# Optimization experiments

Measured on AMD Instinct MI355X. Metric: run time of the kernel, lower is better.

Reference implementation:

```python
import jax, jax.numpy as jnp
import numpy as np

M = 4096  # rows (axis -2), cosine transform axis
N = 4096  # cols (axis -1), sine transform axis


def setup_inputs() -> dict:
    key = jax.random.key(0)
    x = jax.random.normal(key, (M, N), dtype=jnp.float32)
    return {"x": x}


def _cos_basis(n):
    # C[u, p] = cos(pi * (2u+1) * p / (2n))  -- IDXCT basis (no coefficient normalization)
    u = jnp.arange(n, dtype=jnp.float32)
    p = jnp.arange(n, dtype=jnp.float32)
    return jnp.cos(jnp.pi * (2.0 * u[:, None] + 1.0) * p[None, :] / (2.0 * n))


def _sin_basis(n):
    # S[v, q] = sin(pi * (2v+1) * q / (2n))  -- IDXST basis (q=0 column is zero)
    v = jnp.arange(n, dtype=jnp.float32)
    q = jnp.arange(n, dtype=jnp.float32)
    return jnp.sin(jnp.pi * (2.0 * v[:, None] + 1.0) * q[None, :] / (2.0 * n))


def reference(x):
    # idcst2(x) = idxct(idxst(x)^T)^T
    # y_{u,v} = sum_p sum_q x_{p,q} * cos(pi*p*(2u+1)/(2M)) * sin(pi*q*(2v+1)/(2N))
    m, n = x.shape[-2], x.shape[-1]
    C0 = _cos_basis(m).astype(x.dtype)  # [M, M]
    S1 = _sin_basis(n).astype(x.dtype)  # [N, N]
    y = jnp.matmul(x, S1.T)   # IDXST along last axis: [M, N]
    out = jnp.matmul(C0, y)   # IDXCT along axis -2:  [M, N]
    return out
```

## Files before the change

### kernel.cpp

```cpp
#include <hip/hip_runtime.h>


#define NF 4096
#define TWOPI_16384 3.8349519697141029e-4f
#define TWOPI_4096  1.5339807878856412e-3f
#define TWOPI_256   2.4543692606170259e-2f

__device__ __forceinline__ float2 cmul(float2 a, float2 b) {
    return make_float2(a.x * b.x - a.y * b.y, a.x * b.y + a.y * b.x);
}
__device__ __forceinline__ float2 cadd(float2 a, float2 b) {
    return make_float2(a.x + b.x, a.y + b.y);
}
__device__ __forceinline__ float2 csub(float2 a, float2 b) {
    return make_float2(a.x - b.x, a.y - b.y);
}
__device__ __forceinline__ float2 muli(float2 a) {
    return make_float2(-a.y, a.x);
}

__device__ __forceinline__ void fft16(float2 f[16]) {
    float2 s[16];
#pragma unroll
    for (int b = 0; b < 4; ++b) {
        float2 x0 = f[b], x1 = f[b + 4], x2 = f[b + 8], x3 = f[b + 12];
        float2 t0 = cadd(x0, x2), t1 = csub(x0, x2);
        float2 t2 = cadd(x1, x3), t3 = csub(x1, x3);
        s[b]      = cadd(t0, t2);
        s[4 + b]  = cadd(t1, muli(t3));
        s[8 + b]  = csub(t0, t2);
        s[12 + b] = csub(t1, muli(t3));
    }
    const float2 w1 = make_float2(0.92387953251128674f, 0.38268343236508977f);
    const float2 w2 = make_float2(0.70710678118654752f, 0.70710678118654752f);
    const float2 w3 = make_float2(0.38268343236508977f, 0.92387953251128674f);
    const float2 w6 = make_float2(-0.70710678118654752f, 0.70710678118654752f);
    const float2 w9 = make_float2(-0.92387953251128674f, -0.38268343236508977f);
    s[5]  = cmul(s[5], w1);
    s[6]  = cmul(s[6], w2);
    s[7]  = cmul(s[7], w3);
    s[9]  = cmul(s[9], w2);
    s[10] = muli(s[10]);
    s[11] = cmul(s[11], w6);
    s[13] = cmul(s[13], w3);
    s[14] = cmul(s[14], w6);
    s[15] = cmul(s[15], w9);
#pragma unroll
    for (int al = 0; al < 4; ++al) {
        float2 x0 = s[4 * al + 0], x1 = s[4 * al + 1];
        float2 x2 = s[4 * al + 2], x3 = s[4 * al + 3];
        float2 t0 = cadd(x0, x2), t1 = csub(x0, x2);
        float2 t2 = cadd(x1, x3), t3 = csub(x1, x3);
        f[al]      = cadd(t0, t2);
        f[4 + al]  = cadd(t1, muli(t3));
        f[8 + al]  = csub(t0, t2);
        f[12 + al] = csub(t1, muli(t3));
    }
}

__device__ __forceinline__ void fft4096_r16(float2* __restrict__ buf, const int t) {
    float2 r[16];
#pragma unroll
    for (int i = 0; i < 16; ++i) r[i] = buf[i * 256 + t];
    fft16(r);
    {
        float sn, cs;
        __sincosf((float)t * TWOPI_4096, &sn, &cs);
        const float2 wb = make_float2(cs, sn);
        float2 w = wb;
#pragma unroll
        for (int k1 = 1; k1 < 16; ++k1) { r[k1] = cmul(r[k1], w); w = cmul(w, wb); }
    }
#pragma unroll
    for (int i = 0; i < 16; ++i) buf[i * 256 + t] = r[i];
    __syncthreads();
    {
        const int k1 = t >> 4, m2 = t & 15;
        const int base = k1 * 256 + m2;
#pragma unroll
        for (int i = 0; i < 16; ++i) r[i] = buf[base + i * 16];
        fft16(r);
        float sn, cs;
        __sincosf((float)m2 * TWOPI_256, &sn, &cs);
        const float2 wb = make_float2(cs, sn);
        float2 w = wb;
#pragma unroll
        for (int j1 = 1; j1 < 16; ++j1) { r[j1] = cmul(r[j1], w); w = cmul(w, wb); }
        __syncthreads();
        const int bw = k1 * 256 + (m2 ^ k1);
#pragma unroll
        for (int j1 = 0; j1 < 16; ++j1) buf[bw + j1 * 16] = r[j1];
    }
    __syncthreads();
    {
        const int k1 = t & 15;
        const int bc = k1 * 256 + (t >> 4) * 16;
#pragma unroll
        for (int i = 0; i < 16; ++i) r[i] = buf[bc + (i ^ k1)];
        fft16(r);
        __syncthreads();
#pragma unroll
        for (int j2 = 0; j2 < 16; ++j2) buf[j2 * 256 + t] = r[j2];
    }
    __syncthreads();
}

__global__ __launch_bounds__(256) void dst_rows_k(const float* __restrict__ x,
                                                  float* __restrict__ y) {
    __shared__ float2 buf[4096];
    const int t = threadIdx.x;
    const size_t r0 = (size_t)blockIdx.x * 2;
    const float* x0 = x + r0 * NF;
    const float* x1 = x0 + NF;

    float sn, cs;
    __sincosf((float)t * TWOPI_16384, &sn, &cs);
    float2 w = make_float2(cs, sn);
    const float2 stp = make_float2(0.99518472667219693f, 0.09801714032956060f);
#pragma unroll
    for (int v = 0; v < 16; ++v) {
        const int k = t + 256 * v;
        float2 ww = make_float2(0.f, 0.f);
        if (k > 0) {
            float re = x0[NF - k] + x1[k];
            float im = x1[NF - k] - x0[k];
            ww = make_float2(re * w.x - im * w.y, re * w.y + im * w.x);
        }
        buf[k] = ww;
        w = cmul(w, stp);
    }

    fft4096_r16(buf, t);

    float* y0 = y + r0 * NF;
    float* y1 = y0 + NF;
#pragma unroll
    for (int u = 0; u < 8; ++u) {
        const int n = t + 256 * u;
        float2 vn = buf[n];
        float2 vm = buf[NF - 1 - n];
        ((float2*)y0)[n] = make_float2(0.5f * vn.x, -0.5f * vm.x);
        ((float2*)y1)[n] = make_float2(0.5f * vn.y, -0.5f * vm.y);
    }
}

__global__ __launch_bounds__(256) void dct_rows_k(const float* __restrict__ yt,
                                                  float* __restrict__ ot) {
    __shared__ float2 buf[4096];
    const int t = threadIdx.x;
    const size_t r0 = (size_t)blockIdx.x * 2;
    const float* t0 = yt + r0 * NF;
    const float* t1 = t0 + NF;
    const float a0 = t0[0];
    const float a1 = t1[0];

    float sn, cs;
    __sincosf((float)t * TWOPI_16384, &sn, &cs);
    float2 w = make_float2(cs, sn);
    const float2 stp = make_float2(0.99518472667219693f, 0.09801714032956060f);
#pragma unroll
    for (int v = 0; v < 16; ++v) {
        const int k = t + 256 * v;
        float2 ww;
        if (k == 0) {
            ww = make_float2(a0, a1);
        } else {
            float re = t0[k] + t1[NF - k];
            float im = t1[k] - t0[NF - k];
            ww = make_float2(re * w.x - im * w.y, re * w.y + im * w.x);
        }
        buf[k] = ww;
        w = cmul(w, stp);
    }

    fft4096_r16(buf, t);

    float* o0 = ot + r0 * NF;
    float* o1 = o0 + NF;
#pragma unroll
    for (int u = 0; u < 8; ++u) {
        const int n = t + 256 * u;
        float2 vn = buf[n];
        float2 vm = buf[NF - 1 - n];
        ((float2*)o0)[n] = make_float2(0.5f * (vn.x + a0), 0.5f * (vm.x + a0));
        ((float2*)o1)[n] = make_float2(0.5f * (vn.y + a1), 0.5f * (vm.y + a1));
    }
}

__global__ __launch_bounds__(256) void transpose_k(const float* __restrict__ in,
                                                   float* __restrict__ out) {
    __shared__ float tile[32][33];
    const int tx = threadIdx.x;
    const int ty = threadIdx.y;
    const int c0 = blockIdx.x * 32;
    const int r0 = blockIdx.y * 32;

    float4 v = *(const float4*)(in + (size_t)(r0 + ty) * NF + c0 + 4 * tx);
    tile[ty][4 * tx + 0] = v.x;
    tile[ty][4 * tx + 1] = v.y;
    tile[ty][4 * tx + 2] = v.z;
    tile[ty][4 * tx + 3] = v.w;
    __syncthreads();

    float4 o;
    o.x = tile[4 * tx + 0][ty];
    o.y = tile[4 * tx + 1][ty];
    o.z = tile[4 * tx + 2][ty];
    o.w = tile[4 * tx + 3][ty];
    *(float4*)(out + (size_t)(c0 + ty) * NF + r0 + 4 * tx) = o;
}

extern "C" void kernel_launch(void* const* d_in, const int* in_sizes, int n_in,
                              void* d_out, int out_size, void* d_ws, size_t ws_size,
                              hipStream_t stream) {
    const float* x = (const float*)d_in[0];
    float* out = (float*)d_out;
    float* y = (float*)d_ws;

    dim3 tgrid(128, 128), tblk(8, 32);

    dst_rows_k<<<2048, 256, 0, stream>>>(x, y);
    transpose_k<<<tgrid, tblk, 0, stream>>>(y, out);
    dct_rows_k<<<2048, 256, 0, stream>>>(out, y);
    transpose_k<<<tgrid, tblk, 0, stream>>>(y, out);
}
```

Baseline: 183.0 us.

## Fuse transposes into FFT kernels via strided panel stores and reads

Removes both standalone transpose kernels. The DST kernel writes its results column-wise into an interleaved panel layout, and the DCT kernel reads that layout and scatters its output directly into transposed positions. The preprocessing output now stays in registers for the first FFT pass instead of round-tripping through shared memory, and the 0.5 scaling is folded into the twiddles. Block indices are swizzled to group strided writes. The cost is poorly coalesced global stores (8- or 16-byte scattered writes at large strides), traded against removing two full-matrix read-write passes.

After: 214.2 us. +17.1%, slower.

```diff
diff --git a/kernel.cpp b/kernel.cpp
--- a/kernel.cpp
+++ b/kernel.cpp
@@ -58,21 +58,21 @@
     }
 }
 
-__device__ __forceinline__ void fft4096_r16(float2* __restrict__ buf, const int t) {
+__device__ __forceinline__ void fftA_store(float2 r[16], float2* __restrict__ buf,
+                                           const int t) {
+    fft16(r);
+    float sn, cs;
+    __sincosf((float)t * TWOPI_4096, &sn, &cs);
+    const float2 wb = make_float2(cs, sn);
+    float2 w = wb;
+#pragma unroll
+    for (int k1 = 1; k1 < 16; ++k1) { r[k1] = cmul(r[k1], w); w = cmul(w, wb); }
+#pragma unroll
+    for (int i = 0; i < 16; ++i) buf[i * 256 + t] = r[i];
+}
+
+__device__ __forceinline__ void fft4096_tail(float2* __restrict__ buf, const int t) {
     float2 r[16];
-#pragma unroll
-    for (int i = 0; i < 16; ++i) r[i] = buf[i * 256 + t];
-    fft16(r);
-    {
-        float sn, cs;
-        __sincosf((float)t * TWOPI_4096, &sn, &cs);
-        const float2 wb = make_float2(cs, sn);
-        float2 w = wb;
-#pragma unroll
-        for (int k1 = 1; k1 < 16; ++k1) { r[k1] = cmul(r[k1], w); w = cmul(w, wb); }
-    }
-#pragma unroll
-    for (int i = 0; i < 16; ++i) buf[i * 256 + t] = r[i];
     __syncthreads();
     {
         const int k1 = t >> 4, m2 = t & 15;
@@ -105,109 +105,89 @@
     __syncthreads();
 }
 
-__global__ __launch_bounds__(256) void dst_rows_k(const float* __restrict__ x,
-                                                  float* __restrict__ y) {
+__global__ __launch_bounds__(256, 4) void dst_panel_k(const float* __restrict__ x,
+                                                      float* __restrict__ z) {
     __shared__ float2 buf[4096];
     const int t = threadIdx.x;
-    const size_t r0 = (size_t)blockIdx.x * 2;
-    const float* x0 = x + r0 * NF;
+    const int h = blockIdx.x;
+    const int l = (h & 7) * 256 + (h >> 3);
+    const int p0 = 2 * l;
+    const float* x0 = x + (size_t)p0 * NF;
     const float* x1 = x0 + NF;
 
     float sn, cs;
     __sincosf((float)t * TWOPI_16384, &sn, &cs);
-    float2 w = make_float2(cs, sn);
+    float2 w = make_float2(0.5f * cs, 0.5f * sn);
     const float2 stp = make_float2(0.99518472667219693f, 0.09801714032956060f);
-#pragma unroll
-    for (int v = 0; v < 16; ++v) {
-        const int k = t + 256 * v;
+    float2 r[16];
+#pragma unroll
+    for (int i = 0; i < 16; ++i) {
+        const int k = t + 256 * i;
         float2 ww = make_float2(0.f, 0.f);
         if (k > 0) {
             float re = x0[NF - k] + x1[k];
             float im = x1[NF - k] - x0[k];
             ww = make_float2(re * w.x - im * w.y, re * w.y + im * w.x);
         }
-        buf[k] = ww;
+        r[i] = ww;
         w = cmul(w, stp);
     }
-
-    fft4096_r16(buf, t);
-
-    float* y0 = y + r0 * NF;
-    float* y1 = y0 + NF;
+    fftA_store(r, buf, t);
+    fft4096_tail(buf, t);
+
 #pragma unroll
     for (int u = 0; u < 8; ++u) {
         const int n = t + 256 * u;
         float2 vn = buf[n];
         float2 vm = buf[NF - 1 - n];
-        ((float2*)y0)[n] = make_float2(0.5f * vn.x, -0.5f * vm.x);
-        ((float2*)y1)[n] = make_float2(0.5f * vn.y, -0.5f * vm.y);
-    }
-}
-
-__global__ __launch_bounds__(256) void dct_rows_k(const float* __restrict__ yt,
-                                                  float* __restrict__ ot) {
+        float4 q = make_float4(vn.x, -vm.x, vn.y, -vm.y);
+        *(float4*)(z + (size_t)n * 8192 + 2 * p0) = q;
+    }
+}
+
+__global__ __launch_bounds__(256, 4) void dct_panel_k(const float* __restrict__ z,
+                                                      float* __restrict__ out) {
     __shared__ float2 buf[4096];
     const int t = threadIdx.x;
-    const size_t r0 = (size_t)blockIdx.x * 2;
-    const float* t0 = yt + r0 * NF;
-    const float* t1 = t0 + NF;
-    const float a0 = t0[0];
-    const float a1 = t1[0];
+    const int h = blockIdx.x;
+    const int l = (h & 7) * 256 + (h >> 3);
+    const float* pz = z + (size_t)l * 8192;
+    const float a0h = 0.5f * pz[0];
+    const float a1h = 0.5f * pz[1];
 
     float sn, cs;
     __sincosf((float)t * TWOPI_16384, &sn, &cs);
-    float2 w = make_float2(cs, sn);
+    float2 w = make_float2(0.5f * cs, 0.5f * sn);
     const float2 stp = make_float2(0.99518472667219693f, 0.09801714032956060f);
-#pragma unroll
-    for (int v = 0; v < 16; ++v) {
-        const int k = t + 256 * v;
-        float2 ww;
+    float2 r[16];
+#pragma unroll
+    for (int i = 0; i < 16; ++i) {
+        const int k = t + 256 * i;
         if (k == 0) {
-            ww = make_float2(a0, a1);
+            r[i] = make_float2(a0h, a1h);
         } else {
-            float re = t0[k] + t1[NF - k];
-            float im = t1[k] - t0[NF - k];
-            ww = make_float2(re * w.x - im * w.y, re * w.y + im * w.x);
+            float2 f = *(const float2*)(pz + 2 * k);
+            float2 g = *(const float2*)(pz + 2 * (NF - k));
+            float re = f.x + g.y;
+            float im = f.y - g.x;
+            r[i] = make_float2(re * w.x - im * w.y, re * w.y + im * w.x);
         }
-        buf[k] = ww;
         w = cmul(w, stp);
     }
-
-    fft4096_r16(buf, t);
-
-    float* o0 = ot + r0 * NF;
-    float* o1 = o0 + NF;
+    fftA_store(r, buf, t);
+    fft4096_tail(buf, t);
+
+    const int v0 = 2 * l;
 #pragma unroll
     for (int u = 0; u < 8; ++u) {
         const int n = t + 256 * u;
         float2 vn = buf[n];
         float2 vm = buf[NF - 1 - n];
-        ((float2*)o0)[n] = make_float2(0.5f * (vn.x + a0), 0.5f * (vm.x + a0));
-        ((float2*)o1)[n] = make_float2(0.5f * (vn.y + a1), 0.5f * (vm.y + a1));
-    }
-}
-
-__global__ __launch_bounds__(256) void transpose_k(const float* __restrict__ in,
-                                                   float* __restrict__ out) {
-    __shared__ float tile[32][33];
-    const int tx = threadIdx.x;
-    const int ty = threadIdx.y;
-    const int c0 = blockIdx.x * 32;
-    const int r0 = blockIdx.y * 32;
-
-    float4 v = *(const float4*)(in + (size_t)(r0 + ty) * NF + c0 + 4 * tx);
-    tile[ty][4 * tx + 0] = v.x;
-    tile[ty][4 * tx + 1] = v.y;
-    tile[ty][4 * tx + 2] = v.z;
-    tile[ty][4 * tx + 3] = v.w;
-    __syncthreads();
-
-    float4 o;
-    o.x = tile[4 * tx + 0][ty];
-    o.y = tile[4 * tx + 1][ty];
-    o.z = tile[4 * tx + 2][ty];
-    o.w = tile[4 * tx + 3][ty];
-    *(float4*)(out + (size_t)(c0 + ty) * NF + r0 + 4 * tx) = o;
+        *(float2*)(out + (size_t)(2 * n) * NF + v0) =
+            make_float2(vn.x + a0h, vn.y + a1h);
+        *(float2*)(out + (size_t)(2 * n + 1) * NF + v0) =
+            make_float2(vm.x + a0h, vm.y + a1h);
+    }
 }
 
 extern "C" void kernel_launch(void* const* d_in, const int* in_sizes, int n_in,
@@ -215,12 +195,8 @@
                               hipStream_t stream) {
     const float* x = (const float*)d_in[0];
     float* out = (float*)d_out;
-    float* y = (float*)d_ws;
-
-    dim3 tgrid(128, 128), tblk(8, 32);
-
-    dst_rows_k<<<2048, 256, 0, stream>>>(x, y);
-    transpose_k<<<tgrid, tblk, 0, stream>>>(y, out);
-    dct_rows_k<<<2048, 256, 0, stream>>>(out, y);
-    transpose_k<<<tgrid, tblk, 0, stream>>>(y, out);
-}
+    float* z = (float*)d_ws;
+
+    dst_panel_k<<<2048, 256, 0, stream>>>(x, z);
+    dct_panel_k<<<2048, 256, 0, stream>>>(z, out);
+}
```
